# Optimization experiments

Measured on AMD Instinct MI355X. Metric: run time of the kernel, lower is better.

## Reference

```python
import jax, jax.numpy as jnp
import numpy as np

N_NODES = 100000
N_EDGES = 3200000
D = 128
BN_EPS = 1e-5


def setup_inputs() -> dict:
    key = jax.random.key(0)
    k1, k2, k3, k4 = jax.random.split(key, 4)
    x = jax.random.normal(k1, (N_NODES, D), dtype=jnp.float32)
    edge_index = jax.random.randint(k2, (2, N_EDGES), 0, N_NODES, dtype=jnp.int64)
    # GCNConv linear weight, torch nn.Linear convention: [out_dim, in_dim]
    W = jax.random.normal(k3, (D, D), dtype=jnp.float32) * (1.0 / np.sqrt(D))
    # BatchNorm1d affine params
    gamma = jnp.ones((D,), dtype=jnp.float32) + 0.1 * jax.random.normal(k4, (D,), dtype=jnp.float32)
    beta = jnp.zeros((D,), dtype=jnp.float32)
    return {"x": x, "edge_index": edge_index, "W": W, "gamma": gamma, "beta": beta}


def reference(x, edge_index, W, gamma, beta):
    # GCNConv(bias=False, add_self_loops=False), then BN (batch stats), ReLU, skip-add.
    src, dst = edge_index[0], edge_index[1]
    n = x.shape[0]

    # linear transform: [N, D_out]
    h = x @ W.T

    # symmetric GCN normalization: deg over destination, norm = d^-1/2[src]*d^-1/2[dst]
    ones = jnp.ones((src.shape[0],), dtype=x.dtype)
    deg = jax.ops.segment_sum(ones, dst, num_segments=n)
    dinv = jnp.where(deg > 0, jax.lax.rsqrt(jnp.maximum(deg, 1.0)), 0.0)
    norm = dinv[src] * dinv[dst]  # [E]

    # gather-message-scatter: [E, D] -> [N, D]
    msg = h[src] * norm[:, None]
    agg = jax.ops.segment_sum(msg, dst, num_segments=n)

    # BatchNorm1d in training mode (batch statistics, biased variance)
    mean = jnp.mean(agg, axis=0)
    var = jnp.mean(jnp.square(agg - mean), axis=0)
    bn = (agg - mean) * jax.lax.rsqrt(var + BN_EPS) * gamma + beta

    # ReLU + residual skip (dims match)
    out = jax.nn.relu(bn) + x
    return out
```

## Files before the change

kernel.cpp:

```cpp
#include <hip/hip_runtime.h>
#include <hip/hip_bf16.h>
#include <cstdint>
#include <cstddef>

#define D 128
#define SBLK 512
#define SBBITS 8
#define NSB2 512
#define TILE 2048

typedef __attribute__((ext_vector_type(8))) short short8;
typedef __attribute__((ext_vector_type(4))) float f32x4;

__device__ __forceinline__ unsigned short f2bf(float f) {
    union { float f; unsigned u; } v; v.f = f;
    unsigned r = v.u + 0x7FFF + ((v.u >> 16) & 1);
    return (unsigned short)(r >> 16);
}
__device__ __forceinline__ float bflo(unsigned p) {
    union { unsigned u; float f; } v; v.u = p << 16; return v.f;
}
__device__ __forceinline__ float bfhi(unsigned p) {
    union { unsigned u; float f; } v; v.u = p & 0xFFFF0000u; return v.f;
}

__global__ __launch_bounds__(256) void k_prep(const unsigned* __restrict__ ei, int E,
                                              int* __restrict__ flag,
                                              const float* __restrict__ W,
                                              unsigned short* __restrict__ Wbf,
                                              int* __restrict__ g_sbcnt) {
    int t = threadIdx.x, b = blockIdx.x;
    int i = b * 256 + t;
    if (i < D * D) Wbf[i] = f2bf(W[i]);
    if (b == 0 && t == 0) {
        int n = E < 256 ? E : 256;
        int allz = 1;
        for (int k = 0; k < n; ++k) {
            if (ei[2 * k + 1] != 0u) { allz = 0; break; }
        }
        *flag = allz;
    }
    if (b == 63) { g_sbcnt[t] = 0; g_sbcnt[t + 256] = 0; }
}

__global__ __launch_bounds__(256) void k_gemm(const float* __restrict__ x,
                                              const unsigned short* __restrict__ Wbf,
                                              unsigned short* __restrict__ h, int M) {
    int wave = threadIdx.x >> 6, lane = threadIdx.x & 63;
    int m0 = blockIdx.x * 64 + wave * 16;
    int lr = lane & 15;
    int lg = lane >> 4;
    f32x4 acc[8];
#pragma unroll
    for (int i = 0; i < 8; ++i) acc[i] = (f32x4){0.f, 0.f, 0.f, 0.f};

    int row = m0 + lr;
    int rowc = row < M ? row : M - 1;
    const float* xr = x + (size_t)rowc * D;

#pragma unroll
    for (int ks = 0; ks < 4; ++ks) {
        int k0 = ks * 32 + lg * 8;
        float4 a0 = *(const float4*)(xr + k0);
        float4 a1 = *(const float4*)(xr + k0 + 4);
        short8 af;
        af[0] = (short)f2bf(a0.x); af[1] = (short)f2bf(a0.y);
        af[2] = (short)f2bf(a0.z); af[3] = (short)f2bf(a0.w);
        af[4] = (short)f2bf(a1.x); af[5] = (short)f2bf(a1.y);
        af[6] = (short)f2bf(a1.z); af[7] = (short)f2bf(a1.w);
#pragma unroll
        for (int nt = 0; nt < 8; ++nt) {
            short8 bf = *(const short8*)(Wbf + (size_t)(nt * 16 + lr) * D + k0);
            acc[nt] = __builtin_amdgcn_mfma_f32_16x16x32_bf16(af, bf, acc[nt], 0, 0, 0);
        }
    }
#pragma unroll
    for (int nt = 0; nt < 8; ++nt) {
#pragma unroll
        for (int r = 0; r < 4; ++r) {
            int rr = m0 + lg * 4 + r;
            if (rr < M) h[(size_t)rr * D + nt * 16 + lr] = f2bf(acc[nt][r]);
        }
    }
}

__global__ __launch_bounds__(256) void k_bin(const int* __restrict__ ei, int E,
                                             const int* __restrict__ flagp,
                                             int* __restrict__ g_sbcnt,
                                             unsigned* __restrict__ binned, int C2) {
    __shared__ unsigned stage[TILE];
    __shared__ unsigned short ssb[TILE];
    __shared__ int hcnt[NSB2], hoff[NSB2], lcur[NSB2], gbase[NSB2];
    __shared__ int cpair[256];
    int f64 = *flagp;
    int t = threadIdx.x;
    int base = blockIdx.x * TILE;
    int cnt = E - base; if (cnt > TILE) cnt = TILE;

    hcnt[t] = 0; hcnt[t + 256] = 0;
    __syncthreads();

    unsigned ent[8]; int esb[8];
#pragma unroll
    for (int j = 0; j < 8; ++j) {
        int idx = j * 256 + t;
        esb[j] = -1;
        if (idx < cnt) {
            int e = base + idx;
            int s, d;
            if (f64) { s = ei[2 * e]; d = ei[2 * (E + e)]; }
            else     { s = ei[e];     d = ei[E + e]; }
            esb[j] = d >> SBBITS;
            ent[j] = (unsigned)s | ((unsigned)(d & ((1 << SBBITS) - 1)) << 17);
            atomicAdd(&hcnt[esb[j]], 1);
        }
    }
    __syncthreads();
    cpair[t] = hcnt[2 * t] + hcnt[2 * t + 1];
    __syncthreads();
#pragma unroll
    for (int off = 1; off < 256; off <<= 1) {
        int a = (t >= off) ? cpair[t - off] : 0;
        __syncthreads();
        cpair[t] += a;
        __syncthreads();
    }
    {
        int pairsum = hcnt[2 * t] + hcnt[2 * t + 1];
        int ex2 = cpair[t] - pairsum;
        hoff[2 * t] = ex2;
        hoff[2 * t + 1] = ex2 + hcnt[2 * t];
        lcur[2 * t] = ex2;
        lcur[2 * t + 1] = ex2 + hcnt[2 * t];
        gbase[2 * t]     = hcnt[2 * t]     > 0 ? atomicAdd(&g_sbcnt[2 * t],     hcnt[2 * t])     : 0;
        gbase[2 * t + 1] = hcnt[2 * t + 1] > 0 ? atomicAdd(&g_sbcnt[2 * t + 1], hcnt[2 * t + 1]) : 0;
    }
    __syncthreads();
#pragma unroll
    for (int j = 0; j < 8; ++j) {
        if (esb[j] >= 0) {
            int p = atomicAdd(&lcur[esb[j]], 1);
            stage[p] = ent[j];
            ssb[p] = (unsigned short)esb[j];
        }
    }
    __syncthreads();
    for (int i = t; i < cnt; i += 256) {
        int sb = ssb[i];
        int pos = gbase[sb] + (i - hoff[sb]);
        if (pos < C2) binned[(size_t)sb * C2 + pos] = stage[i];
    }
}

__global__ __launch_bounds__(256) void k_fill2(const unsigned* __restrict__ binned, int C2,
                                               const int* __restrict__ g_sbcnt,
                                               int2* __restrict__ ronode,
                                               float* __restrict__ dinv,
                                               int* __restrict__ csrc, int N) {
    __shared__ int deg[256];
    __shared__ int scn[256];
    __shared__ int cur[256];
    int b = blockIdx.x, t = threadIdx.x;
    int cnt = g_sbcnt[b]; if (cnt > C2) cnt = C2;
    const unsigned* ent = binned + (size_t)b * C2;

    deg[t] = 0;
    __syncthreads();
    for (int i = t; i < cnt; i += 256) atomicAdd(&deg[ent[i] >> 17], 1);
    __syncthreads();
    scn[t] = deg[t];
    __syncthreads();
#pragma unroll
    for (int off = 1; off < 256; off <<= 1) {
        int a = (t >= off) ? scn[t - off] : 0;
        __syncthreads();
        scn[t] += a;
        __syncthreads();
    }
    int ex = scn[t] - deg[t];
    cur[t] = ex;
    int node = (b << SBBITS) + t;
    if (node < N) {
        ronode[node] = make_int2(b * C2 + ex, deg[t]);
        dinv[node] = deg[t] > 0 ? rsqrtf((float)deg[t]) : 0.0f;
    }
    __syncthreads();
    for (int i = t; i < cnt; i += 256) {
        unsigned e = ent[i];
        int pos = atomicAdd(&cur[e >> 17], 1);
        csrc[b * C2 + pos] = (int)(e & 0x1FFFF);
    }
}

__global__ __launch_bounds__(256) void k_agg(const unsigned long long* __restrict__ h,
                                             const int* __restrict__ csrc,
                                             const int2* __restrict__ ronode,
                                             const float* __restrict__ dinv,
                                             float4* __restrict__ out, int N) {
    int wave = threadIdx.x >> 6, lane = threadIdx.x & 63;
    int node = blockIdx.x * 4 + wave;
    if (node >= N) return;
    int half = lane >> 5, lq = lane & 31;
    int2 ro = ronode[node];
    int beg = ro.x, end = ro.x + ro.y;
    float a0 = 0.f, a1 = 0.f, a2 = 0.f, a3 = 0.f;
    int i = beg;
    for (; i + 16 <= end; i += 16) {
#pragma unroll
        for (int p = 0; p < 8; ++p) {
            int e = i + 2 * p + half;
            int s = csrc[e];
            float w = dinv[s];
            unsigned long long pk = h[(size_t)s * 32 + lq];
            unsigned lo = (unsigned)pk, hi = (unsigned)(pk >> 32);
            a0 += w * bflo(lo); a1 += w * bfhi(lo);
            a2 += w * bflo(hi); a3 += w * bfhi(hi);
        }
    }
    for (; i + 2 <= end; i += 2) {
        int e = i + half;
        int s = csrc[e];
        float w = dinv[s];
        unsigned long long pk = h[(size_t)s * 32 + lq];
        unsigned lo = (unsigned)pk, hi = (unsigned)(pk >> 32);
        a0 += w * bflo(lo); a1 += w * bfhi(lo);
        a2 += w * bflo(hi); a3 += w * bfhi(hi);
    }
    if (i < end) {
        int s = csrc[i];
        float w = half ? 0.f : dinv[s];
        unsigned long long pk = h[(size_t)s * 32 + lq];
        unsigned lo = (unsigned)pk, hi = (unsigned)(pk >> 32);
        a0 += w * bflo(lo); a1 += w * bfhi(lo);
        a2 += w * bflo(hi); a3 += w * bfhi(hi);
    }
    a0 += __shfl_xor(a0, 32);
    a1 += __shfl_xor(a1, 32);
    a2 += __shfl_xor(a2, 32);
    a3 += __shfl_xor(a3, 32);
    float sd = dinv[node];
    if (half == 0)
        out[(size_t)node * 32 + lq] = make_float4(a0 * sd, a1 * sd, a2 * sd, a3 * sd);
}

__global__ __launch_bounds__(256) void k_stats(const float* __restrict__ agg,
                                               float* __restrict__ part, int N) {
    int t = threadIdx.x;
    int c = t & 127, half = t >> 7;
    float s = 0.f, q = 0.f;
    for (int r = blockIdx.x * 2 + half; r < N; r += SBLK * 2) {
        float v = agg[(size_t)r * 128 + c];
        s += v; q += v * v;
    }
    __shared__ float sh[512];
    sh[t] = s; sh[256 + t] = q;
    __syncthreads();
    if (t < 128) {
        part[blockIdx.x * 256 + t]       = sh[t] + sh[t + 128];
        part[blockIdx.x * 256 + 128 + t] = sh[256 + t] + sh[256 + t + 128];
    }
}

__global__ void k_params(const float* __restrict__ part, const float* __restrict__ gamma,
                         const float* __restrict__ beta, float* __restrict__ params, int N) {
    int t = threadIdx.x;
    float a = 0.f;
    for (int b = 0; b < SBLK; ++b) a += part[b * 256 + t];
    __shared__ float sh[256];
    sh[t] = a;
    __syncthreads();
    if (t < 128) {
        float mean = sh[t] / (float)N;
        float var = sh[128 + t] / (float)N - mean * mean;
        var = var > 0.f ? var : 0.f;
        float sc = gamma[t] * rsqrtf(var + 1e-5f);
        params[t] = sc;
        params[128 + t] = beta[t] - mean * sc;
    }
}

__global__ __launch_bounds__(256) void k_final(float4* __restrict__ out,
                                               const float4* __restrict__ x,
                                               const float* __restrict__ params, int n4) {
    const float4* p4 = (const float4*)params;
    for (int i = blockIdx.x * 256 + threadIdx.x; i < n4; i += gridDim.x * 256) {
        int c = i & 31;
        float4 s = p4[c], b = p4[32 + c];
        float4 v = out[i], xv = x[i];
        float4 r;
        r.x = fmaxf(v.x * s.x + b.x, 0.f) + xv.x;
        r.y = fmaxf(v.y * s.y + b.y, 0.f) + xv.y;
        r.z = fmaxf(v.z * s.z + b.z, 0.f) + xv.z;
        r.w = fmaxf(v.w * s.w + b.w, 0.f) + xv.w;
        out[i] = r;
    }
}

extern "C" void kernel_launch(void* const* d_in, const int* in_sizes, int n_in,
                              void* d_out, int out_size, void* d_ws, size_t ws_size,
                              hipStream_t stream) {
    const float* x     = (const float*)d_in[0];
    const int*   ei    = (const int*)d_in[1];
    const float* W     = (const float*)d_in[2];
    const float* gamma = (const float*)d_in[3];
    const float* beta  = (const float*)d_in[4];

    int N = in_sizes[0] / D;
    int E = in_sizes[1] / 2;
    int NSBu = (N + (1 << SBBITS) - 1) >> SBBITS;
    int avg = (E + NSBu - 1) / NSBu;
    int C2 = ((avg + 1024 + 63) / 64) * 64;

    char* ws = (char*)d_ws;
    size_t off = 0;
    auto alloc = [&](size_t bytes) { size_t o = off; off = (off + bytes + 255) & ~(size_t)255; return o; };

    unsigned short* h    = (unsigned short*)(ws + alloc((size_t)N * D * 2));
    int*      csrc   = (int*)     (ws + alloc((size_t)NSBu * C2 * 4));
    unsigned* binned = (unsigned*)(ws + alloc((size_t)NSBu * C2 * 4));
    int*      g_sbcnt= (int*)     (ws + alloc((size_t)NSB2 * 4));
    float*    dinv   = (float*)   (ws + alloc((size_t)N * 4));
    int2*     ronode = (int2*)    (ws + alloc((size_t)N * 8));
    float*    part   = (float*)   (ws + alloc((size_t)SBLK * 256 * 4));
    float*    params = (float*)   (ws + alloc(256 * 4));
    int*      flagp  = (int*)     (ws + alloc(4));
    unsigned short* Wbf = (unsigned short*)(ws + alloc((size_t)D * D * 2));

    float* outf = (float*)d_out;

    k_prep<<<64, 256, 0, stream>>>((const unsigned*)ei, E, flagp, W, Wbf, g_sbcnt);
    k_gemm<<<(N + 63) / 64, 256, 0, stream>>>(x, Wbf, h, N);
    k_bin<<<(E + TILE - 1) / TILE, 256, 0, stream>>>(ei, E, flagp, g_sbcnt, binned, C2);
    k_fill2<<<NSBu, 256, 0, stream>>>(binned, C2, g_sbcnt, ronode, dinv, csrc, N);
    k_agg<<<(N + 3) / 4, 256, 0, stream>>>((const unsigned long long*)h, csrc, ronode, dinv,
                                           (float4*)d_out, N);
    k_stats<<<SBLK, 256, 0, stream>>>(outf, part, N);
    k_params<<<1, 256, 0, stream>>>(part, gamma, beta, params, N);
    k_final<<<2048, 256, 0, stream>>>((float4*)d_out, (const float4*)x, params,
                                      (N * D) / 4);
}
```

Baseline: 413.8 us.

## Fuse BN statistics into aggregation and coarsen destination binning

```diff
diff --git a/kernel.cpp b/kernel.cpp
--- a/kernel.cpp
+++ b/kernel.cpp
@@ -4,10 +4,11 @@
 #include <cstddef>
 
 #define D 128
-#define SBLK 512
-#define SBBITS 8
-#define NSB2 512
-#define TILE 2048
+#define SBBITS 10
+#define NSB 128
+#define TILE 4096
+#define BINT 512
+#define NSLOT 64
 
 typedef __attribute__((ext_vector_type(8))) short short8;
 typedef __attribute__((ext_vector_type(4))) float f32x4;
@@ -28,10 +29,12 @@
                                               int* __restrict__ flag,
                                               const float* __restrict__ W,
                                               unsigned short* __restrict__ Wbf,
-                                              int* __restrict__ g_sbcnt) {
+                                              int* __restrict__ g_sbcnt,
+                                              float* __restrict__ part2) {
     int t = threadIdx.x, b = blockIdx.x;
     int i = b * 256 + t;
     if (i < D * D) Wbf[i] = f2bf(W[i]);
+    part2[i] = 0.f;
     if (b == 0 && t == 0) {
         int n = E < 256 ? E : 256;
         int allz = 1;
@@ -40,7 +43,7 @@
         }
         *flag = allz;
     }
-    if (b == 63) { g_sbcnt[t] = 0; g_sbcnt[t + 256] = 0; }
+    if (b == 63 && t < NSB) g_sbcnt[t] = 0;
 }
 
 __global__ __launch_bounds__(256) void k_gemm(const float* __restrict__ x,
@@ -84,26 +87,25 @@
     }
 }
 
-__global__ __launch_bounds__(256) void k_bin(const int* __restrict__ ei, int E,
-                                             const int* __restrict__ flagp,
-                                             int* __restrict__ g_sbcnt,
-                                             unsigned* __restrict__ binned, int C2) {
+__global__ __launch_bounds__(BINT) void k_bin(const int* __restrict__ ei, int E,
+                                              const int* __restrict__ flagp,
+                                              int* __restrict__ g_sbcnt,
+                                              unsigned* __restrict__ binned, int C2) {
     __shared__ unsigned stage[TILE];
-    __shared__ unsigned short ssb[TILE];
-    __shared__ int hcnt[NSB2], hoff[NSB2], lcur[NSB2], gbase[NSB2];
-    __shared__ int cpair[256];
+    __shared__ unsigned char ssb[TILE];
+    __shared__ int hcnt[NSB], hoff[NSB], lcur[NSB], gbase[NSB];
     int f64 = *flagp;
     int t = threadIdx.x;
     int base = blockIdx.x * TILE;
     int cnt = E - base; if (cnt > TILE) cnt = TILE;
 
-    hcnt[t] = 0; hcnt[t + 256] = 0;
+    if (t < NSB) hcnt[t] = 0;
     __syncthreads();
 
     unsigned ent[8]; int esb[8];
 #pragma unroll
     for (int j = 0; j < 8; ++j) {
-        int idx = j * 256 + t;
+        int idx = j * BINT + t;
         esb[j] = -1;
         if (idx < cnt) {
             int e = base + idx;
@@ -116,24 +118,20 @@
         }
     }
     __syncthreads();
-    cpair[t] = hcnt[2 * t] + hcnt[2 * t + 1];
-    __syncthreads();
-#pragma unroll
-    for (int off = 1; off < 256; off <<= 1) {
-        int a = (t >= off) ? cpair[t - off] : 0;
+    if (t < NSB) hoff[t] = hcnt[t];
+    __syncthreads();
+#pragma unroll
+    for (int off = 1; off < NSB; off <<= 1) {
+        int a = (t < NSB && t >= off) ? hoff[t - off] : 0;
         __syncthreads();
-        cpair[t] += a;
+        if (t < NSB) hoff[t] += a;
         __syncthreads();
     }
-    {
-        int pairsum = hcnt[2 * t] + hcnt[2 * t + 1];
-        int ex2 = cpair[t] - pairsum;
-        hoff[2 * t] = ex2;
-        hoff[2 * t + 1] = ex2 + hcnt[2 * t];
-        lcur[2 * t] = ex2;
-        lcur[2 * t + 1] = ex2 + hcnt[2 * t];
-        gbase[2 * t]     = hcnt[2 * t]     > 0 ? atomicAdd(&g_sbcnt[2 * t],     hcnt[2 * t])     : 0;
-        gbase[2 * t + 1] = hcnt[2 * t + 1] > 0 ? atomicAdd(&g_sbcnt[2 * t + 1], hcnt[2 * t + 1]) : 0;
+    if (t < NSB) {
+        int ex = hoff[t] - hcnt[t];
+        lcur[t] = ex;
+        hoff[t] = ex;
+        gbase[t] = (hcnt[t] > 0) ? atomicAdd(&g_sbcnt[t], hcnt[t]) : 0;
     }
     __syncthreads();
 #pragma unroll
@@ -141,37 +139,36 @@
         if (esb[j] >= 0) {
             int p = atomicAdd(&lcur[esb[j]], 1);
             stage[p] = ent[j];
-            ssb[p] = (unsigned short)esb[j];
-        }
-    }
-    __syncthreads();
-    for (int i = t; i < cnt; i += 256) {
+            ssb[p] = (unsigned char)esb[j];
+        }
+    }
+    __syncthreads();
+    for (int i = t; i < cnt; i += BINT) {
         int sb = ssb[i];
         int pos = gbase[sb] + (i - hoff[sb]);
         if (pos < C2) binned[(size_t)sb * C2 + pos] = stage[i];
     }
 }
 
-__global__ __launch_bounds__(256) void k_fill2(const unsigned* __restrict__ binned, int C2,
-                                               const int* __restrict__ g_sbcnt,
-                                               int2* __restrict__ ronode,
-                                               float* __restrict__ dinv,
-                                               int* __restrict__ csrc, int N) {
-    __shared__ int deg[256];
-    __shared__ int scn[256];
-    __shared__ int cur[256];
+__global__ __launch_bounds__(1024) void k_fill2(const unsigned* __restrict__ binned, int C2,
+                                                const int* __restrict__ g_sbcnt,
+                                                int2* __restrict__ ronode,
+                                                float* __restrict__ dinv,
+                                                int* __restrict__ csrc, int N) {
+    __shared__ int deg[1024];
+    __shared__ int scn[1024];
+    __shared__ int cur[1024];
     int b = blockIdx.x, t = threadIdx.x;
     int cnt = g_sbcnt[b]; if (cnt > C2) cnt = C2;
     const unsigned* ent = binned + (size_t)b * C2;
 
     deg[t] = 0;
     __syncthreads();
-    for (int i = t; i < cnt; i += 256) atomicAdd(&deg[ent[i] >> 17], 1);
+    for (int i = t; i < cnt; i += 1024) atomicAdd(&deg[ent[i] >> 17], 1);
     __syncthreads();
     scn[t] = deg[t];
     __syncthreads();
-#pragma unroll
-    for (int off = 1; off < 256; off <<= 1) {
+    for (int off = 1; off < 1024; off <<= 1) {
         int a = (t >= off) ? scn[t - off] : 0;
         __syncthreads();
         scn[t] += a;
@@ -185,7 +182,7 @@
         dinv[node] = deg[t] > 0 ? rsqrtf((float)deg[t]) : 0.0f;
     }
     __syncthreads();
-    for (int i = t; i < cnt; i += 256) {
+    for (int i = t; i < cnt; i += 1024) {
         unsigned e = ent[i];
         int pos = atomicAdd(&cur[e >> 17], 1);
         csrc[b * C2 + pos] = (int)(e & 0x1FFFF);
@@ -196,19 +193,36 @@
                                              const int* __restrict__ csrc,
                                              const int2* __restrict__ ronode,
                                              const float* __restrict__ dinv,
-                                             float4* __restrict__ out, int N) {
-    int wave = threadIdx.x >> 6, lane = threadIdx.x & 63;
+                                             float4* __restrict__ out,
+                                             float* __restrict__ part2, int N) {
+    __shared__ float ssum[128], ssq[128];
+    int t = threadIdx.x;
+    int wave = t >> 6, lane = t & 63;
     int node = blockIdx.x * 4 + wave;
-    if (node >= N) return;
     int half = lane >> 5, lq = lane & 31;
-    int2 ro = ronode[node];
-    int beg = ro.x, end = ro.x + ro.y;
-    float a0 = 0.f, a1 = 0.f, a2 = 0.f, a3 = 0.f;
-    int i = beg;
-    for (; i + 16 <= end; i += 16) {
-#pragma unroll
-        for (int p = 0; p < 8; ++p) {
-            int e = i + 2 * p + half;
+    if (t < 128) { ssum[t] = 0.f; ssq[t] = 0.f; }
+    __syncthreads();
+
+    float v0 = 0.f, v1 = 0.f, v2 = 0.f, v3 = 0.f;
+    if (node < N) {
+        int2 ro = ronode[node];
+        int beg = ro.x, end = ro.x + ro.y;
+        float a0 = 0.f, a1 = 0.f, a2 = 0.f, a3 = 0.f;
+        int i = beg;
+        for (; i + 16 <= end; i += 16) {
+#pragma unroll
+            for (int p = 0; p < 8; ++p) {
+                int e = i + 2 * p + half;
+                int s = csrc[e];
+                float w = dinv[s];
+                unsigned long long pk = h[(size_t)s * 32 + lq];
+                unsigned lo = (unsigned)pk, hi = (unsigned)(pk >> 32);
+                a0 += w * bflo(lo); a1 += w * bfhi(lo);
+                a2 += w * bflo(hi); a3 += w * bfhi(hi);
+            }
+        }
+        for (; i + 2 <= end; i += 2) {
+            int e = i + half;
             int s = csrc[e];
             float w = dinv[s];
             unsigned long long pk = h[(size_t)s * 32 + lq];
@@ -216,56 +230,40 @@
             a0 += w * bflo(lo); a1 += w * bfhi(lo);
             a2 += w * bflo(hi); a3 += w * bfhi(hi);
         }
-    }
-    for (; i + 2 <= end; i += 2) {
-        int e = i + half;
-        int s = csrc[e];
-        float w = dinv[s];
-        unsigned long long pk = h[(size_t)s * 32 + lq];
-        unsigned lo = (unsigned)pk, hi = (unsigned)(pk >> 32);
-        a0 += w * bflo(lo); a1 += w * bfhi(lo);
-        a2 += w * bflo(hi); a3 += w * bfhi(hi);
-    }
-    if (i < end) {
-        int s = csrc[i];
-        float w = half ? 0.f : dinv[s];
-        unsigned long long pk = h[(size_t)s * 32 + lq];
-        unsigned lo = (unsigned)pk, hi = (unsigned)(pk >> 32);
-        a0 += w * bflo(lo); a1 += w * bfhi(lo);
-        a2 += w * bflo(hi); a3 += w * bfhi(hi);
-    }
-    a0 += __shfl_xor(a0, 32);
-    a1 += __shfl_xor(a1, 32);
-    a2 += __shfl_xor(a2, 32);
-    a3 += __shfl_xor(a3, 32);
-    float sd = dinv[node];
-    if (half == 0)
-        out[(size_t)node * 32 + lq] = make_float4(a0 * sd, a1 * sd, a2 * sd, a3 * sd);
-}
-
-__global__ __launch_bounds__(256) void k_stats(const float* __restrict__ agg,
-                                               float* __restrict__ part, int N) {
-    int t = threadIdx.x;
-    int c = t & 127, half = t >> 7;
-    float s = 0.f, q = 0.f;
-    for (int r = blockIdx.x * 2 + half; r < N; r += SBLK * 2) {
-        float v = agg[(size_t)r * 128 + c];
-        s += v; q += v * v;
-    }
-    __shared__ float sh[512];
-    sh[t] = s; sh[256 + t] = q;
-    __syncthreads();
-    if (t < 128) {
-        part[blockIdx.x * 256 + t]       = sh[t] + sh[t + 128];
-        part[blockIdx.x * 256 + 128 + t] = sh[256 + t] + sh[256 + t + 128];
-    }
-}
-
-__global__ void k_params(const float* __restrict__ part, const float* __restrict__ gamma,
+        if (i < end) {
+            int s = csrc[i];
+            float w = half ? 0.f : dinv[s];
+            unsigned long long pk = h[(size_t)s * 32 + lq];
+            unsigned lo = (unsigned)pk, hi = (unsigned)(pk >> 32);
+            a0 += w * bflo(lo); a1 += w * bfhi(lo);
+            a2 += w * bflo(hi); a3 += w * bfhi(hi);
+        }
+        a0 += __shfl_xor(a0, 32);
+        a1 += __shfl_xor(a1, 32);
+        a2 += __shfl_xor(a2, 32);
+        a3 += __shfl_xor(a3, 32);
+        float sd = dinv[node];
+        v0 = a0 * sd; v1 = a1 * sd; v2 = a2 * sd; v3 = a3 * sd;
+        if (half == 0) {
+            out[(size_t)node * 32 + lq] = make_float4(v0, v1, v2, v3);
+            int c = lq * 4;
+            atomicAdd(&ssum[c],     v0); atomicAdd(&ssq[c],     v0 * v0);
+            atomicAdd(&ssum[c + 1], v1); atomicAdd(&ssq[c + 1], v1 * v1);
+            atomicAdd(&ssum[c + 2], v2); atomicAdd(&ssq[c + 2], v2 * v2);
+            atomicAdd(&ssum[c + 3], v3); atomicAdd(&ssq[c + 3], v3 * v3);
+        }
+    }
+    __syncthreads();
+    int slot = blockIdx.x & (NSLOT - 1);
+    if (t < 128)            atomicAdd(&part2[slot * 256 + t],       ssum[t]);
+    else if (t < 256)       atomicAdd(&part2[slot * 256 + t],       ssq[t - 128]);
+}
+
+__global__ void k_params(const float* __restrict__ part2, const float* __restrict__ gamma,
                          const float* __restrict__ beta, float* __restrict__ params, int N) {
     int t = threadIdx.x;
     float a = 0.f;
-    for (int b = 0; b < SBLK; ++b) a += part[b * 256 + t];
+    for (int s = 0; s < NSLOT; ++s) a += part2[s * 256 + t];
     __shared__ float sh[256];
     sh[t] = a;
     __syncthreads();
@@ -309,7 +307,7 @@
     int E = in_sizes[1] / 2;
     int NSBu = (N + (1 << SBBITS) - 1) >> SBBITS;
     int avg = (E + NSBu - 1) / NSBu;
-    int C2 = ((avg + 1024 + 63) / 64) * 64;
+    int C2 = ((avg + 4096 + 63) / 64) * 64;
 
     char* ws = (char*)d_ws;
     size_t off = 0;
@@ -318,24 +316,21 @@
     unsigned short* h    = (unsigned short*)(ws + alloc((size_t)N * D * 2));
     int*      csrc   = (int*)     (ws + alloc((size_t)NSBu * C2 * 4));
     unsigned* binned = (unsigned*)(ws + alloc((size_t)NSBu * C2 * 4));
-    int*      g_sbcnt= (int*)     (ws + alloc((size_t)NSB2 * 4));
+    int*      g_sbcnt= (int*)     (ws + alloc((size_t)NSB * 4));
     float*    dinv   = (float*)   (ws + alloc((size_t)N * 4));
     int2*     ronode = (int2*)    (ws + alloc((size_t)N * 8));
-    float*    part   = (float*)   (ws + alloc((size_t)SBLK * 256 * 4));
+    float*    part2  = (float*)   (ws + alloc((size_t)NSLOT * 256 * 4));
     float*    params = (float*)   (ws + alloc(256 * 4));
     int*      flagp  = (int*)     (ws + alloc(4));
     unsigned short* Wbf = (unsigned short*)(ws + alloc((size_t)D * D * 2));
 
-    float* outf = (float*)d_out;
-
-    k_prep<<<64, 256, 0, stream>>>((const unsigned*)ei, E, flagp, W, Wbf, g_sbcnt);
+    k_prep<<<64, 256, 0, stream>>>((const unsigned*)ei, E, flagp, W, Wbf, g_sbcnt, part2);
     k_gemm<<<(N + 63) / 64, 256, 0, stream>>>(x, Wbf, h, N);
-    k_bin<<<(E + TILE - 1) / TILE, 256, 0, stream>>>(ei, E, flagp, g_sbcnt, binned, C2);
-    k_fill2<<<NSBu, 256, 0, stream>>>(binned, C2, g_sbcnt, ronode, dinv, csrc, N);
+    k_bin<<<(E + TILE - 1) / TILE, BINT, 0, stream>>>(ei, E, flagp, g_sbcnt, binned, C2);
+    k_fill2<<<NSBu, 1024, 0, stream>>>(binned, C2, g_sbcnt, ronode, dinv, csrc, N);
     k_agg<<<(N + 3) / 4, 256, 0, stream>>>((const unsigned long long*)h, csrc, ronode, dinv,
-                                           (float4*)d_out, N);
-    k_stats<<<SBLK, 256, 0, stream>>>(outf, part, N);
-    k_params<<<1, 256, 0, stream>>>(part, gamma, beta, params, N);
+                                           (float4*)d_out, part2, N);
+    k_params<<<1, 256, 0, stream>>>(part2, gamma, beta, params, N);
     k_final<<<2048, 256, 0, stream>>>((float4*)d_out, (const float4*)x, params,
                                       (N * D) / 4);
 }
```

Result: slower. 422.2 us (+2.0%).
